# Kernel optimization log

Measured on AMD Instinct MI355X. Metric: run time of the kernel, lower is better.

## Reference

```python
import jax, jax.numpy as jnp
import numpy as np
import math

D_MODEL = 1024
EXPAND = 2
D_INNER = EXPAND * D_MODEL  # 2048
D_STATE = 16
D_CONV = 4
DT_RANK = math.ceil(D_MODEL / 16)  # 64
BATCH = 1
SEQLEN = 2048


def _silu(x):
    return x * jax.nn.sigmoid(x)


def _selective_scan(u, delta, A, B, C, D, z, delta_bias):
    """u, delta, z: (b,d,l); A: (d,n); B, C: (b,n,l); D, delta_bias: (d)."""
    delta = jax.nn.softplus(delta + delta_bias[None, :, None])        # (b,d,l)
    dA = jnp.exp(jnp.einsum('bdl,dn->lbdn', delta, A))                # (l,b,d,n)
    dBu = jnp.einsum('bdl,bnl->lbdn', delta * u, B)                   # (l,b,d,n)
    Ct = jnp.transpose(C, (2, 0, 1))                                  # (l,b,n)

    def step(h, inp):
        dA_t, dBu_t, C_t = inp
        h = dA_t * h + dBu_t                                          # (b,d,n)
        y = jnp.einsum('bdn,bn->bd', h, C_t)
        return h, y

    h0 = jnp.zeros((u.shape[0], u.shape[1], A.shape[1]), dtype=u.dtype)
    _, ys = jax.lax.scan(step, h0, (dA, dBu, Ct))                     # ys: (l,b,d)
    y = jnp.transpose(ys, (1, 2, 0))                                  # (b,d,l)
    y = y + D[:, None] * u
    return y * _silu(z)


def _causal_conv1d(x, conv_w, conv_b):
    """x: (b,d,l); conv_w: (d,w); conv_b: (d). Depthwise causal conv."""
    x_pad = jnp.pad(x, ((0, 0), (0, 0), (D_CONV - 1, 0)))
    kernel = conv_w[:, None, :]  # (d, 1, w)
    y = jax.lax.conv_general_dilated(
        x_pad, kernel, window_strides=(1,), padding='VALID',
        dimension_numbers=('NCH', 'OIH', 'NCH'),
        feature_group_count=D_INNER)
    return y + conv_b[None, :, None]


def setup_inputs() -> dict:
    key = jax.random.key(0)
    ks = jax.random.split(key, 12)
    hidden_states = jax.random.normal(ks[0], (BATCH, SEQLEN, D_MODEL), dtype=jnp.float32)
    in_proj_w = jax.random.normal(ks[1], (2 * D_INNER, D_MODEL), dtype=jnp.float32) * (D_MODEL ** -0.5)
    conv_w = jax.random.normal(ks[2], (D_INNER, D_CONV), dtype=jnp.float32) * (D_CONV ** -0.5)
    conv_b = jnp.zeros((D_INNER,), dtype=jnp.float32)
    dt_std = DT_RANK ** -0.5

    def dt_bias(k):
        dt = jnp.exp(jax.random.uniform(k, (D_INNER,)) * (math.log(0.1) - math.log(0.001)) + math.log(0.001))
        dt = jnp.clip(dt, 1e-4, None)
        return dt + jnp.log(-jnp.expm1(-dt))  # inverse softplus

    A_log = jnp.log(jnp.broadcast_to(jnp.arange(1, D_STATE + 1, dtype=jnp.float32), (D_INNER, D_STATE)))
    x1_proj_w = jax.random.normal(ks[3], (DT_RANK + 2 * D_STATE, D_INNER), dtype=jnp.float32) * (D_INNER ** -0.5)
    dt1_proj_w = jax.random.uniform(ks[4], (D_INNER, DT_RANK), minval=-dt_std, maxval=dt_std)
    dt1_proj_b = dt_bias(ks[5])
    x2_proj_w = jax.random.normal(ks[6], (DT_RANK + 2 * D_STATE, D_INNER), dtype=jnp.float32) * (D_INNER ** -0.5)
    dt2_proj_w = jax.random.uniform(ks[7], (D_INNER, DT_RANK), minval=-dt_std, maxval=dt_std)
    dt2_proj_b = dt_bias(ks[8])
    out_proj_w = jax.random.normal(ks[9], (D_MODEL, D_INNER), dtype=jnp.float32) * (D_INNER ** -0.5)
    return {
        'hidden_states': hidden_states,
        'in_proj_w': in_proj_w, 'conv_w': conv_w, 'conv_b': conv_b,
        'x1_proj_w': x1_proj_w, 'dt1_proj_w': dt1_proj_w, 'dt1_proj_b': dt1_proj_b,
        'A1_log': A_log, 'D1': jnp.ones((D_INNER,), dtype=jnp.float32),
        'x2_proj_w': x2_proj_w, 'dt2_proj_w': dt2_proj_w, 'dt2_proj_b': dt2_proj_b,
        'A2_log': A_log, 'D2': jnp.ones((D_INNER,), dtype=jnp.float32),
        'out_proj_w': out_proj_w,
    }


def reference(hidden_states, in_proj_w, conv_w, conv_b,
              x1_proj_w, dt1_proj_w, dt1_proj_b, A1_log, D1,
              x2_proj_w, dt2_proj_w, dt2_proj_b, A2_log, D2,
              out_proj_w):
    # in_proj: (b,l,d) @ W^T -> (b, 2*d_inner, l)
    xz = jnp.einsum('bld,ed->bel', hidden_states, in_proj_w)
    x, z = jnp.split(xz, 2, axis=1)                                   # (b,d_inner,l) each
    A1 = -jnp.exp(A1_log.astype(jnp.float32))
    A2 = -jnp.exp(A2_log.astype(jnp.float32))
    x = _silu(_causal_conv1d(x, conv_w, conv_b))                      # (b,d_inner,l)

    def branch_params(xp_w, dtp_w):
        dbl = jnp.einsum('bdl,kd->bkl', x, xp_w)                      # (b, r+2n, l)
        dt, Bm, Cm = jnp.split(dbl, [DT_RANK, DT_RANK + D_STATE], axis=1)
        dt = jnp.einsum('brl,dr->bdl', dt, dtp_w)
        return dt, Bm, Cm

    dt1, B1, C1 = branch_params(x1_proj_w, dt1_proj_w)
    dt2, B2, C2 = branch_params(x2_proj_w, dt2_proj_w)
    y1 = _selective_scan(x, dt1, A1, B1, C1, D1.astype(jnp.float32), z, dt1_proj_b.astype(jnp.float32))
    y2 = _selective_scan(x, dt2, A2, B2, C2, D2.astype(jnp.float32), z, dt2_proj_b.astype(jnp.float32))
    y = y1 - y2                                                       # (b,d_inner,l)
    out = jnp.einsum('bdl,od->blo', y, out_proj_w)                    # (b,l,d_model)
    return out
```

## Files before the change

kernel.cpp:

```cpp
#include <hip/hip_runtime.h>
#include <math.h>

#define SEQ 2048
#define DMODEL 1024
#define DIN 2048
#define NST 16
#define DTR 64
#define CH 64
#define NCH (SEQ / CH)

typedef __attribute__((ext_vector_type(8))) short bf16x8;
typedef __attribute__((ext_vector_type(4))) float f32x4;

__device__ __forceinline__ ushort f2bf(float f) {
  union { float f; unsigned u; } c; c.f = f;
  return (ushort)((c.u + 0x7fffu + ((c.u >> 16) & 1u)) >> 16);
}
__device__ __forceinline__ float bf2f(ushort h) {
  union { unsigned u; float f; } c; c.u = ((unsigned)h) << 16;
  return c.f;
}
__device__ __forceinline__ float splus(float v) {
  return v > 20.f ? v : log1pf(__expf(v));
}
__device__ __forceinline__ void powers16(float e, float* p) {
  float e2 = e * e, e4 = e2 * e2, e8 = e4 * e4;
  p[0] = e;       p[1] = e2;       p[2] = e2 * e;   p[3] = e4;
  p[4] = e4 * e;  p[5] = e4 * e2;  p[6] = e4 * p[2]; p[7] = e8;
  p[8] = e8 * e;  p[9] = e8 * e2;  p[10] = e8 * p[2]; p[11] = e8 * e4;
  p[12] = e8 * p[4]; p[13] = e8 * p[5]; p[14] = e8 * p[6]; p[15] = e8 * e8;
}

#define GLL(g, l) __builtin_amdgcn_global_load_lds( \
    (const __attribute__((address_space(1))) void*)(g), \
    (__attribute__((address_space(3))) void*)(l), 16, 0, 0)

template<int BM, int BN, int SPLITK, int MODE>
__global__ __launch_bounds__(256) void gemm3p(const ushort* __restrict__ Ahi,
                                              const ushort* __restrict__ Alo,
                                              const ushort* __restrict__ Bhi,
                                              const ushort* __restrict__ Blo,
                                              float* __restrict__ C,
                                              int M, int N, int K) {
  constexpr int BK = 32;
  constexpr int WM = BM / 2, WN = BN / 2, TM = WM / 16, TN = WN / 16;
  constexpr int SA = BM / 16, SB = BN / 16;
  constexpr bool dropB = (MODE == 2);
  __shared__ __align__(16) ushort sAh[BM * BK], sAl[BM * BK];
  __shared__ __align__(16) ushort sBh[BN * BK], sBl[BN * BK];
  const int tid = threadIdx.x, wid = tid >> 6, lane = tid & 63;
  const int m0 = blockIdx.y * BM, n0 = blockIdx.x * BN;
  const int Kc = K / SPLITK, kbeg = blockIdx.z * Kc;
  const int wm0 = (wid >> 1) * WM, wn0 = (wid & 1) * WN;
  const int fr = lane & 15;
  const int lrow = lane >> 2;
  const int lkc = (lane & 3) ^ ((lane >> 3) & 3);
  const int fpo = fr * 32 + (((lane >> 4) ^ ((lane >> 1) & 3)) * 8);

  f32x4 acc[TM][TN];
#pragma unroll
  for (int mi = 0; mi < TM; ++mi)
#pragma unroll
    for (int ni = 0; ni < TN; ++ni)
#pragma unroll
      for (int r = 0; r < 4; ++r) acc[mi][ni][r] = 0.f;

  for (int k0 = 0; k0 < Kc; k0 += BK) {
    __syncthreads();
    const int kg = kbeg + k0 + lkc * 8;
#pragma unroll
    for (int i = 0; i < SA / 4; ++i) {
      const int seg = wid * (SA / 4) + i;
      const size_t ga = (size_t)(m0 + seg * 16 + lrow) * K + kg;
      GLL(&Ahi[ga], &sAh[seg * 512]);
      GLL(&Alo[ga], &sAl[seg * 512]);
    }
#pragma unroll
    for (int i = 0; i < SB / 4; ++i) {
      const int seg = wid * (SB / 4) + i;
      const size_t ga = (size_t)(n0 + seg * 16 + lrow) * K + kg;
      GLL(&Bhi[ga], &sBh[seg * 512]);
      if (!dropB) GLL(&Blo[ga], &sBl[seg * 512]);
    }
    __syncthreads();

    bf16x8 ah[TM], al[TM], bh[TN], bl[TN];
#pragma unroll
    for (int mi = 0; mi < TM; ++mi) {
      const int r = (wm0 / 16 + mi) * 512 + fpo;
      ah[mi] = *(const bf16x8*)&sAh[r];
      al[mi] = *(const bf16x8*)&sAl[r];
    }
#pragma unroll
    for (int ni = 0; ni < TN; ++ni) {
      const int r = (wn0 / 16 + ni) * 512 + fpo;
      bh[ni] = *(const bf16x8*)&sBh[r];
      if (!dropB) bl[ni] = *(const bf16x8*)&sBl[r];
    }
#pragma unroll
    for (int mi = 0; mi < TM; ++mi)
#pragma unroll
      for (int ni = 0; ni < TN; ++ni) {
        acc[mi][ni] = __builtin_amdgcn_mfma_f32_16x16x32_bf16(ah[mi], bh[ni], acc[mi][ni], 0, 0, 0);
        if (!dropB)
          acc[mi][ni] = __builtin_amdgcn_mfma_f32_16x16x32_bf16(ah[mi], bl[ni], acc[mi][ni], 0, 0, 0);
        acc[mi][ni] = __builtin_amdgcn_mfma_f32_16x16x32_bf16(al[mi], bh[ni], acc[mi][ni], 0, 0, 0);
      }
  }

  float* __restrict__ Co = C + (size_t)blockIdx.z * M * N;
#pragma unroll
  for (int mi = 0; mi < TM; ++mi)
#pragma unroll
    for (int ni = 0; ni < TN; ++ni)
#pragma unroll
      for (int r = 0; r < 4; ++r)
        Co[(size_t)(m0 + wm0 + mi * 16 + (lane >> 4) * 4 + r) * N + n0 + wn0 + ni * 16 + fr] =
            acc[mi][ni][r];
}

__device__ __forceinline__ void split_store4(float4 v, ushort* hi, ushort* lo, size_t i) {
  ushort h0 = f2bf(v.x), h1 = f2bf(v.y), h2 = f2bf(v.z), h3 = f2bf(v.w);
  *(ushort4*)&hi[i] = make_ushort4(h0, h1, h2, h3);
  *(ushort4*)&lo[i] = make_ushort4(f2bf(v.x - bf2f(h0)), f2bf(v.y - bf2f(h1)),
                                   f2bf(v.z - bf2f(h2)), f2bf(v.w - bf2f(h3)));
}

__global__ __launch_bounds__(256) void cvt_fused(const float* __restrict__ inw,
                                                 const float* __restrict__ hid,
                                                 const float* __restrict__ x1w,
                                                 const float* __restrict__ x2w,
                                                 ushort* __restrict__ w_hi, ushort* __restrict__ w_lo,
                                                 ushort* __restrict__ h_hi, ushort* __restrict__ h_lo,
                                                 ushort* __restrict__ wx_hi, ushort* __restrict__ wx_lo) {
  const int q = blockIdx.x * 256 + threadIdx.x;
  const float* src; ushort* dhi; ushort* dlo; int base;
  if (q < 1048576)            { src = inw; dhi = w_hi;  dlo = w_lo;  base = q; }
  else if (q < 1572864)       { src = hid; dhi = h_hi;  dlo = h_lo;  base = q - 1048576; }
  else if (q < 1622016)       { src = x1w; dhi = wx_hi; dlo = wx_lo; base = q - 1572864; }
  else                        { src = x2w; dhi = wx_hi + 196608; dlo = wx_lo + 196608; base = q - 1622016; }
  const size_t i = (size_t)base * 4;
  split_store4(*(const float4*)&src[i], dhi, dlo, i);
}

__global__ __launch_bounds__(256) void reduce_out(const float* __restrict__ p,
                                                  float* __restrict__ o, int n) {
  const int i = (blockIdx.x * 256 + threadIdx.x) * 4;
  if (i >= n) return;
  float4 a = *(const float4*)&p[i];
  float4 b = *(const float4*)&p[(size_t)n + i];
  float4 c = *(const float4*)&p[(size_t)2 * n + i];
  float4 d = *(const float4*)&p[(size_t)3 * n + i];
  *(float4*)&o[i] = make_float4(a.x + b.x + c.x + d.x, a.y + b.y + c.y + d.y,
                                a.z + b.z + c.z + d.z, a.w + b.w + c.w + d.w);
}

__global__ __launch_bounds__(256) void conv_tr_kernel(const float* __restrict__ xz,
                                                      const float* __restrict__ cw,
                                                      const float* __restrict__ cb,
                                                      ushort* __restrict__ xcT_hi,
                                                      ushort* __restrict__ xcT_lo) {
  const int l0 = blockIdx.x * 64, d0 = blockIdx.y * 64;
  const int tid = threadIdx.x;
  __shared__ float xin[64][68];
  __shared__ float To[64][65];
  __shared__ float cwS[64][4];
  __shared__ float cbS[64];

  for (int i = tid; i < 1024; i += 256) {
    const int d = i >> 4, q = i & 15;
    float4 v = *(const float4*)&xz[(size_t)(d0 + d) * SEQ + l0 + q * 4];
    xin[d][3 + q * 4 + 0] = v.x; xin[d][3 + q * 4 + 1] = v.y;
    xin[d][3 + q * 4 + 2] = v.z; xin[d][3 + q * 4 + 3] = v.w;
  }
  if (tid < 192) {
    const int j = tid >> 6, d = tid & 63;
    const int l = l0 - 3 + j;
    xin[d][j] = (l >= 0) ? xz[(size_t)(d0 + d) * SEQ + l] : 0.f;
  }
  if (tid < 64) {
    cbS[tid] = cb[d0 + tid];
    float4 w = *(const float4*)&cw[(d0 + tid) * 4];
    cwS[tid][0] = w.x; cwS[tid][1] = w.y; cwS[tid][2] = w.z; cwS[tid][3] = w.w;
  }
  __syncthreads();

  for (int i = tid; i < 4096; i += 256) {
    const int d = i >> 6, l = i & 63;
    float a = cbS[d] + cwS[d][0] * xin[d][l] + cwS[d][1] * xin[d][l + 1] +
              cwS[d][2] * xin[d][l + 2] + cwS[d][3] * xin[d][l + 3];
    To[d][l] = a / (1.f + __expf(-a));
  }
  __syncthreads();

  for (int i = tid; i < 4096; i += 256) {
    const int l = i >> 6, dd = i & 63;
    float v = To[dd][l];
    ushort h = f2bf(v);
    xcT_hi[(size_t)(l0 + l) * DIN + d0 + dd] = h;
    xcT_lo[(size_t)(l0 + l) * DIN + d0 + dd] = f2bf(v - bf2f(h));
  }
}

__global__ __launch_bounds__(256) void ydiff_tr_kernel(const float* __restrict__ y1,
                                                       const float* __restrict__ y2,
                                                       const float* __restrict__ xz,
                                                       ushort* __restrict__ hi,
                                                       ushort* __restrict__ lo) {
  const int l0 = blockIdx.x * 64, d0 = blockIdx.y * 64;
  const int tid = threadIdx.x;
  __shared__ float Tz[64][65];
  for (int i = tid; i < 1024; i += 256) {
    const int d = i >> 4, q = i & 15;
    float4 v = *(const float4*)&xz[(size_t)(DIN + d0 + d) * SEQ + l0 + q * 4];
    Tz[d][q * 4 + 0] = v.x / (1.f + __expf(-v.x));
    Tz[d][q * 4 + 1] = v.y / (1.f + __expf(-v.y));
    Tz[d][q * 4 + 2] = v.z / (1.f + __expf(-v.z));
    Tz[d][q * 4 + 3] = v.w / (1.f + __expf(-v.w));
  }
  __syncthreads();
  for (int i = tid; i < 1024; i += 256) {
    const int l = i >> 4, dc = (i & 15) * 4;
    const size_t g = (size_t)(l0 + l) * DIN + d0 + dc;
    float4 a = *(const float4*)&y1[g];
    float4 b = *(const float4*)&y2[g];
    float4 v = make_float4((a.x - b.x) * Tz[dc + 0][l], (a.y - b.y) * Tz[dc + 1][l],
                           (a.z - b.z) * Tz[dc + 2][l], (a.w - b.w) * Tz[dc + 3][l]);
    split_store4(v, hi, lo, g);
  }
}

__global__ __launch_bounds__(256) void reduce_dblS_kernel(const float* __restrict__ p,
                                                          float* __restrict__ o,
                                                          float* __restrict__ BT1,
                                                          float* __restrict__ CT1,
                                                          float* __restrict__ BT2,
                                                          float* __restrict__ CT2) {
  const int NE = 192 * SEQ;
  const int idx = blockIdx.x * 256 + threadIdx.x;
  float s = 0.f;
#pragma unroll
  for (int cc = 0; cc < 8; ++cc) s += p[(size_t)cc * NE + idx];
  o[idx] = s;
  const int k = idx >> 11, l = idx & (SEQ - 1);
  if (k >= 64 && k < 80)        BT1[l * NST + (k - 64)] = s;
  else if (k >= 80 && k < 96)   CT1[l * NST + (k - 80)] = s;
  else if (k >= 160 && k < 176) BT2[l * NST + (k - 160)] = s;
  else if (k >= 176)            CT2[l * NST + (k - 176)] = s;
}

__global__ __launch_bounds__(256) void dt_gemm_kernel(const float* __restrict__ dbl1,
                                                      const float* __restrict__ dbl2,
                                                      const float* __restrict__ w1,
                                                      const float* __restrict__ w2,
                                                      const float* __restrict__ b1,
                                                      const float* __restrict__ b2,
                                                      float* __restrict__ o1,
                                                      float* __restrict__ o2) {
  const int br = blockIdx.z;
  const float* __restrict__ dbl = br ? dbl2 : dbl1;
  const float* __restrict__ W = br ? w2 : w1;
  const float* __restrict__ dtb = br ? b2 : b1;
  float* __restrict__ outp = br ? o2 : o1;
  const int l0 = blockIdx.x * 64, d0 = blockIdx.y * 64;
  __shared__ __align__(16) float Wt[64][68];
  __shared__ __align__(16) float Bs[64][68];
  const int tid = threadIdx.x;
  for (int i = tid; i < 4096; i += 256) {
    int a = i >> 6, b = i & 63;
    Wt[b][a] = W[(size_t)(d0 + a) * DTR + b];
    Bs[a][b] = dbl[(size_t)a * SEQ + l0 + b];
  }
  __syncthreads();
  const int tl_ = tid >> 4, td_ = tid & 15;
  float acc[4][4];
#pragma unroll
  for (int i = 0; i < 4; ++i)
#pragma unroll
    for (int j = 0; j < 4; ++j) acc[i][j] = 0.f;
  for (int r = 0; r < 64; ++r) {
    float4 av = *(const float4*)&Bs[r][tl_ * 4];
    float4 bv = *(const float4*)&Wt[r][td_ * 4];
    float am[4] = {av.x, av.y, av.z, av.w};
    float bn[4] = {bv.x, bv.y, bv.z, bv.w};
#pragma unroll
    for (int i = 0; i < 4; ++i)
#pragma unroll
      for (int j = 0; j < 4; ++j) acc[i][j] = fmaf(am[i], bn[j], acc[i][j]);
  }
  const float4 bias4 = *(const float4*)&dtb[d0 + td_ * 4];
#pragma unroll
  for (int i = 0; i < 4; ++i) {
    float4 w = make_float4(splus(acc[i][0] + bias4.x), splus(acc[i][1] + bias4.y),
                           splus(acc[i][2] + bias4.z), splus(acc[i][3] + bias4.w));
    *(float4*)&outp[(size_t)(l0 + tl_ * 4 + i) * DIN + d0 + td_ * 4] = w;
  }
}

__global__ __launch_bounds__(256) void scan_phase_a(const ushort* __restrict__ uhi,
                                                    const ushort* __restrict__ ulo,
                                                    const float* __restrict__ sp1T,
                                                    const float* __restrict__ sp2T,
                                                    const float* __restrict__ BT1,
                                                    const float* __restrict__ BT2,
                                                    const float* __restrict__ Al1,
                                                    const float* __restrict__ Al2,
                                                    float* __restrict__ hend,
                                                    float* __restrict__ Pend) {
  const int br = blockIdx.z;
  const float* __restrict__ spp = br ? sp2T : sp1T;
  const float* __restrict__ BT = br ? BT2 : BT1;
  const float* __restrict__ Al = br ? Al2 : Al1;
  const int c = blockIdx.y;
  const int t0 = c * CH;
  const int d = blockIdx.x * 256 + threadIdx.x;
  const size_t gbase = (size_t)t0 * DIN + d;

  __shared__ __align__(16) float Bs[CH][NST];
  ((float4*)Bs)[threadIdx.x] = ((const float4*)&BT[t0 * NST])[threadIdx.x];
  __syncthreads();

  bool fast = true;
#pragma unroll
  for (int n = 0; n < NST; ++n) {
    float kx = __expf(Al[(size_t)d * NST + n]);
    fast = fast && (fabsf(kx - (float)(n + 1)) < 1e-3f);
  }
  float h[NST];
#pragma unroll
  for (int n = 0; n < NST; ++n) h[n] = 0.f;
  float S = 0.f;

  if (fast) {
    for (int tt = 0; tt < CH / 4; ++tt) {
      float sparr[4], uarr[4];
#pragma unroll
      for (int j = 0; j < 4; ++j) {
        const size_t idx = gbase + (size_t)(tt * 4 + j) * DIN;
        sparr[j] = spp[idx];
        uarr[j] = bf2f(uhi[idx]) + bf2f(ulo[idx]);
      }
#pragma unroll
      for (int j = 0; j < 4; ++j) {
        const int t = tt * 4 + j;
        const float sp = sparr[j];
        S += sp;
        const float spu = sp * uarr[j];
        const float e = __expf(-sp);
        float p[NST];
        powers16(e, p);
#pragma unroll
        for (int ng = 0; ng < 4; ++ng) {
          float4 bq = *(const float4*)&Bs[t][ng * 4];
          float bf[4] = {bq.x, bq.y, bq.z, bq.w};
#pragma unroll
          for (int k = 0; k < 4; ++k) {
            int n = ng * 4 + k;
            h[n] = fmaf(p[n], h[n], spu * bf[k]);
          }
        }
      }
    }
  } else {
    float AnL2[NST];
#pragma unroll
    for (int n = 0; n < NST; ++n)
      AnL2[n] = -__expf(Al[(size_t)d * NST + n]) * 1.4426950408889634f;
    for (int tt = 0; tt < CH / 4; ++tt) {
      float sparr[4], uarr[4];
#pragma unroll
      for (int j = 0; j < 4; ++j) {
        const size_t idx = gbase + (size_t)(tt * 4 + j) * DIN;
        sparr[j] = spp[idx];
        uarr[j] = bf2f(uhi[idx]) + bf2f(ulo[idx]);
      }
#pragma unroll
      for (int j = 0; j < 4; ++j) {
        const int t = tt * 4 + j;
        const float sp = sparr[j];
        S += sp;
        const float spu = sp * uarr[j];
#pragma unroll
        for (int ng = 0; ng < 4; ++ng) {
          float4 bq = *(const float4*)&Bs[t][ng * 4];
          float bf[4] = {bq.x, bq.y, bq.z, bq.w};
#pragma unroll
          for (int k = 0; k < 4; ++k) {
            int n = ng * 4 + k;
            float dA = exp2f(AnL2[n] * sp);
            h[n] = fmaf(dA, h[n], spu * bf[k]);
          }
        }
      }
    }
  }

  float P[NST];
  if (fast) {
    powers16(__expf(-S), P);
  } else {
#pragma unroll
    for (int n = 0; n < NST; ++n)
      P[n] = exp2f(-__expf(Al[(size_t)d * NST + n]) * 1.4426950408889634f * S);
  }
  size_t base = ((size_t)(br * NCH + c) * DIN + d) * NST;
#pragma unroll
  for (int n = 0; n < NST; n += 4) {
    *(float4*)&hend[base + n] = make_float4(h[n], h[n + 1], h[n + 2], h[n + 3]);
    *(float4*)&Pend[base + n] = make_float4(P[n], P[n + 1], P[n + 2], P[n + 3]);
  }
}

__global__ __launch_bounds__(256) void carry_cvt(const float* __restrict__ hend,
                                                 float* __restrict__ PendHin,
                                                 const float* __restrict__ outw,
                                                 ushort* __restrict__ ow_hi) {
  const int b = blockIdx.x;
  if (b < 256) {
    const int flat = b * 256 + threadIdx.x;
    const int br = flat >> 15;
    const int dn = flat & 32767;
    float h = 0.f;
    for (int c = 0; c < NCH; ++c) {
      size_t idx = ((size_t)(br * NCH + c) << 15) + dn;
      float Pv = PendHin[idx];
      float he = hend[idx];
      PendHin[idx] = h;
      h = fmaf(Pv, h, he);
    }
  } else {
    const size_t i = ((size_t)(b - 256) * 256 + threadIdx.x) * 4;
    float4 v = *(const float4*)&outw[i];
    *(ushort4*)&ow_hi[i] = make_ushort4(f2bf(v.x), f2bf(v.y), f2bf(v.z), f2bf(v.w));
  }
}

__global__ __launch_bounds__(256) void scan_phase_c(const ushort* __restrict__ uhi,
                                                    const ushort* __restrict__ ulo,
                                                    const float* __restrict__ sp1T,
                                                    const float* __restrict__ sp2T,
                                                    const float* __restrict__ BT1,
                                                    const float* __restrict__ CT1,
                                                    const float* __restrict__ BT2,
                                                    const float* __restrict__ CT2,
                                                    const float* __restrict__ Al1,
                                                    const float* __restrict__ Al2,
                                                    const float* __restrict__ D1,
                                                    const float* __restrict__ D2,
                                                    const float* __restrict__ hin,
                                                    float* __restrict__ y1t,
                                                    float* __restrict__ y2t) {
  const int br = blockIdx.z;
  const float* __restrict__ spp = br ? sp2T : sp1T;
  const float* __restrict__ BT = br ? BT2 : BT1;
  const float* __restrict__ CT = br ? CT2 : CT1;
  const float* __restrict__ Al = br ? Al2 : Al1;
  const float* __restrict__ Dp = br ? D2 : D1;
  float* __restrict__ yt = br ? y2t : y1t;
  const int c = blockIdx.y;
  const int t0 = c * CH;
  const int d = blockIdx.x * 256 + threadIdx.x;
  const size_t gbase = (size_t)t0 * DIN + d;

  __shared__ __align__(16) float Bs[CH][NST];
  __shared__ __align__(16) float Cs[CH][NST];
  ((float4*)Bs)[threadIdx.x] = ((const float4*)&BT[t0 * NST])[threadIdx.x];
  ((float4*)Cs)[threadIdx.x] = ((const float4*)&CT[t0 * NST])[threadIdx.x];
  __syncthreads();

  bool fast = true;
#pragma unroll
  for (int n = 0; n < NST; ++n) {
    float kx = __expf(Al[(size_t)d * NST + n]);
    fast = fast && (fabsf(kx - (float)(n + 1)) < 1e-3f);
  }
  const float Dd = Dp[d];
  float h[NST];
  const size_t hbase = ((size_t)(br * NCH + c) * DIN + d) * NST;
#pragma unroll
  for (int n = 0; n < NST; n += 4) {
    float4 hv = *(const float4*)&hin[hbase + n];
    h[n] = hv.x; h[n + 1] = hv.y; h[n + 2] = hv.z; h[n + 3] = hv.w;
  }

  if (fast) {
    for (int tt = 0; tt < CH / 4; ++tt) {
      float sparr[4], uarr[4];
#pragma unroll
      for (int j = 0; j < 4; ++j) {
        const size_t idx = gbase + (size_t)(tt * 4 + j) * DIN;
        sparr[j] = spp[idx];
        uarr[j] = bf2f(uhi[idx]) + bf2f(ulo[idx]);
      }
#pragma unroll
      for (int j = 0; j < 4; ++j) {
        const int t = tt * 4 + j;
        const float sp = sparr[j];
        const float spu = sp * uarr[j];
        const float e = __expf(-sp);
        float p[NST];
        powers16(e, p);
        float y = 0.f;
#pragma unroll
        for (int ng = 0; ng < 4; ++ng) {
          float4 bq = *(const float4*)&Bs[t][ng * 4];
          float4 cq = *(const float4*)&Cs[t][ng * 4];
          float bf[4] = {bq.x, bq.y, bq.z, bq.w};
          float cf[4] = {cq.x, cq.y, cq.z, cq.w};
#pragma unroll
          for (int k = 0; k < 4; ++k) {
            int n = ng * 4 + k;
            h[n] = fmaf(p[n], h[n], spu * bf[k]);
            y = fmaf(h[n], cf[k], y);
          }
        }
        yt[gbase + (size_t)t * DIN] = y + Dd * uarr[j];
      }
    }
  } else {
    float AnL2[NST];
#pragma unroll
    for (int n = 0; n < NST; ++n)
      AnL2[n] = -__expf(Al[(size_t)d * NST + n]) * 1.4426950408889634f;
    for (int tt = 0; tt < CH / 4; ++tt) {
      float sparr[4], uarr[4];
#pragma unroll
      for (int j = 0; j < 4; ++j) {
        const size_t idx = gbase + (size_t)(tt * 4 + j) * DIN;
        sparr[j] = spp[idx];
        uarr[j] = bf2f(uhi[idx]) + bf2f(ulo[idx]);
      }
#pragma unroll
      for (int j = 0; j < 4; ++j) {
        const int t = tt * 4 + j;
        const float sp = sparr[j];
        const float spu = sp * uarr[j];
        float y = 0.f;
#pragma unroll
        for (int ng = 0; ng < 4; ++ng) {
          float4 bq = *(const float4*)&Bs[t][ng * 4];
          float4 cq = *(const float4*)&Cs[t][ng * 4];
          float bf[4] = {bq.x, bq.y, bq.z, bq.w};
          float cf[4] = {cq.x, cq.y, cq.z, cq.w};
#pragma unroll
          for (int k = 0; k < 4; ++k) {
            int n = ng * 4 + k;
            float dA = exp2f(AnL2[n] * sp);
            h[n] = fmaf(dA, h[n], spu * bf[k]);
            y = fmaf(h[n], cf[k], y);
          }
        }
        yt[gbase + (size_t)t * DIN] = y + Dd * uarr[j];
      }
    }
  }
}

extern "C" void kernel_launch(void* const* d_in, const int* in_sizes, int n_in,
                              void* d_out, int out_size, void* d_ws, size_t ws_size,
                              hipStream_t stream) {
  const float* hidden = (const float*)d_in[0];
  const float* in_proj_w = (const float*)d_in[1];
  const float* conv_w = (const float*)d_in[2];
  const float* conv_b = (const float*)d_in[3];
  const float* x1w = (const float*)d_in[4];
  const float* dtw1 = (const float*)d_in[5];
  const float* dtb1 = (const float*)d_in[6];
  const float* Al1 = (const float*)d_in[7];
  const float* D1 = (const float*)d_in[8];
  const float* x2w = (const float*)d_in[9];
  const float* dtw2 = (const float*)d_in[10];
  const float* dtb2 = (const float*)d_in[11];
  const float* Al2 = (const float*)d_in[12];
  const float* D2 = (const float*)d_in[13];
  const float* outw = (const float*)d_in[14];
  float* out = (float*)d_out;

  float* ws = (float*)d_ws;
  float* xz = ws;
  float* xcTbuf = xz + (size_t)4096 * SEQ;
  float* dblS = xcTbuf + (size_t)SEQ * DIN;
  float* sp1T = dblS + (size_t)192 * SEQ;
  float* sp2T = sp1T + (size_t)SEQ * DIN;
  float* y1t = sp2T + (size_t)SEQ * DIN;
  float* y2t = y1t + (size_t)SEQ * DIN;
  float* hend = y2t + (size_t)SEQ * DIN;
  float* Pend = hend + (size_t)2 * NCH * DIN * NST;
  float* BT1 = Pend + (size_t)2 * NCH * DIN * NST;
  float* CT1 = BT1 + (size_t)SEQ * NST;
  float* BT2 = CT1 + (size_t)SEQ * NST;
  float* CT2 = BT2 + (size_t)SEQ * NST;
  float* wxp = CT2 + (size_t)SEQ * NST;

  float* dbl1 = dblS;
  float* dbl2 = dblS + (size_t)96 * SEQ;

  ushort* xcT_hi = (ushort*)xcTbuf;
  ushort* xcT_lo = (ushort*)(xcTbuf + 2097152);
  ushort* w_hi = (ushort*)y1t;
  ushort* w_lo = (ushort*)(y1t + 2097152);
  ushort* h_hi = (ushort*)y2t;
  ushort* h_lo = (ushort*)(y2t + 1048576);
  ushort* wx_hi = (ushort*)wxp;
  ushort* wx_lo = (ushort*)(wxp + 196608);
  float* xp_part = sp1T;
  ushort* yd_hi = (ushort*)xcTbuf;
  ushort* yd_lo = (ushort*)(xcTbuf + 2097152);
  ushort* ow_hi = (ushort*)xz;
  float* opart = sp1T;

  dim3 blk(256);

  cvt_fused<<<dim3(6528), blk, 0, stream>>>(in_proj_w, hidden, x1w, x2w,
                                            w_hi, w_lo, h_hi, h_lo, wx_hi, wx_lo);

  gemm3p<128, 128, 1, 0><<<dim3(SEQ / 128, 4096 / 128, 1), blk, 0, stream>>>(
      w_hi, w_lo, h_hi, h_lo, xz, 4096, SEQ, DMODEL);

  conv_tr_kernel<<<dim3(SEQ / 64, DIN / 64), blk, 0, stream>>>(
      xz, conv_w, conv_b, xcT_hi, xcT_lo);

  gemm3p<64, 128, 8, 0><<<dim3(SEQ / 128, 192 / 64, 8), blk, 0, stream>>>(
      wx_hi, wx_lo, xcT_hi, xcT_lo, xp_part, 192, SEQ, DIN);

  reduce_dblS_kernel<<<dim3(192 * SEQ / 256), blk, 0, stream>>>(
      xp_part, dblS, BT1, CT1, BT2, CT2);

  dt_gemm_kernel<<<dim3(SEQ / 64, DIN / 64, 2), blk, 0, stream>>>(
      dbl1, dbl2, dtw1, dtw2, dtb1, dtb2, sp1T, sp2T);

  scan_phase_a<<<dim3(DIN / 256, NCH, 2), blk, 0, stream>>>(
      xcT_hi, xcT_lo, sp1T, sp2T, BT1, BT2, Al1, Al2, hend, Pend);
  carry_cvt<<<dim3(2304), blk, 0, stream>>>(hend, Pend, outw, ow_hi);
  scan_phase_c<<<dim3(DIN / 256, NCH, 2), blk, 0, stream>>>(
      xcT_hi, xcT_lo, sp1T, sp2T, BT1, CT1, BT2, CT2, Al1, Al2, D1, D2, Pend, y1t, y2t);

  ydiff_tr_kernel<<<dim3(SEQ / 64, DIN / 64), blk, 0, stream>>>(
      y1t, y2t, xz, yd_hi, yd_lo);

  gemm3p<128, 128, 4, 2><<<dim3(DMODEL / 128, SEQ / 128, 4), blk, 0, stream>>>(
      yd_hi, yd_lo, ow_hi, ow_hi, opart, SEQ, DMODEL, DIN);
  reduce_out<<<dim3(SEQ * DMODEL / 1024), blk, 0, stream>>>(opart, out, SEQ * DMODEL);
}
```

Before: 327.1 us.

## Switch split-precision GEMMs to fp16 with scaled residuals and fuse scan branches

Replaces the bf16 hi/lo split with fp16 hi plus a residual scaled by 2048, accumulated separately, and drops the low part of the hidden-state operand in the in_proj GEMM (MODE 2), which removes one MFMA per tile step. It also moves the silu(z) transpose into the conv kernel and fuses both scan branches into one thread, so the y-difference, gating and hi/lo split happen inside scan_phase_c and the ydiff kernel goes away. The scan chunk length is halved to expose more parallelism, and the GEMM gets a launch-bounds occupancy hint. These changes cut kernel launches, memory traffic and MFMA count, but fp16 has a narrower range than bf16 and dropping the activation residual may reduce accuracy.

```diff
diff --git a/kernel.cpp b/kernel.cpp
--- a/kernel.cpp
+++ b/kernel.cpp
@@ -6,19 +6,18 @@
 #define DIN 2048
 #define NST 16
 #define DTR 64
-#define CH 64
+#define CH 32
 #define NCH (SEQ / CH)
-
-typedef __attribute__((ext_vector_type(8))) short bf16x8;
+#define LOG2E 1.4426950408889634f
+
+typedef __attribute__((ext_vector_type(8))) _Float16 f16x8;
 typedef __attribute__((ext_vector_type(4))) float f32x4;
 
-__device__ __forceinline__ ushort f2bf(float f) {
-  union { float f; unsigned u; } c; c.f = f;
-  return (ushort)((c.u + 0x7fffu + ((c.u >> 16) & 1u)) >> 16);
-}
-__device__ __forceinline__ float bf2f(ushort h) {
-  union { unsigned u; float f; } c; c.u = ((unsigned)h) << 16;
-  return c.f;
+__device__ __forceinline__ ushort f2h(float f) {
+  union { _Float16 h; ushort u; } c; c.h = (_Float16)f; return c.u;
+}
+__device__ __forceinline__ float h2f(ushort u) {
+  union { ushort u; _Float16 h; } c; c.u = u; return (float)c.h;
 }
 __device__ __forceinline__ float splus(float v) {
   return v > 20.f ? v : log1pf(__expf(v));
@@ -36,18 +35,19 @@
     (__attribute__((address_space(3))) void*)(l), 16, 0, 0)
 
 template<int BM, int BN, int SPLITK, int MODE>
-__global__ __launch_bounds__(256) void gemm3p(const ushort* __restrict__ Ahi,
-                                              const ushort* __restrict__ Alo,
-                                              const ushort* __restrict__ Bhi,
-                                              const ushort* __restrict__ Blo,
-                                              float* __restrict__ C,
-                                              int M, int N, int K) {
+__global__ __launch_bounds__(256, 2) void gemm3p(const ushort* __restrict__ Ahi,
+                                                 const ushort* __restrict__ Alo,
+                                                 const ushort* __restrict__ Bhi,
+                                                 const ushort* __restrict__ Blo,
+                                                 float* __restrict__ C,
+                                                 int M, int N, int K) {
   constexpr int BK = 32;
   constexpr int WM = BM / 2, WN = BN / 2, TM = WM / 16, TN = WN / 16;
   constexpr int SA = BM / 16, SB = BN / 16;
   constexpr bool dropB = (MODE == 2);
   __shared__ __align__(16) ushort sAh[BM * BK], sAl[BM * BK];
-  __shared__ __align__(16) ushort sBh[BN * BK], sBl[BN * BK];
+  __shared__ __align__(16) ushort sBh[BN * BK];
+  __shared__ __align__(16) ushort sBl[dropB ? 16 : BN * BK];
   const int tid = threadIdx.x, wid = tid >> 6, lane = tid & 63;
   const int m0 = blockIdx.y * BM, n0 = blockIdx.x * BN;
   const int Kc = K / SPLITK, kbeg = blockIdx.z * Kc;
@@ -57,13 +57,13 @@
   const int lkc = (lane & 3) ^ ((lane >> 3) & 3);
   const int fpo = fr * 32 + (((lane >> 4) ^ ((lane >> 1) & 3)) * 8);
 
-  f32x4 acc[TM][TN];
+  f32x4 acc[TM][TN], accL[TM][TN];
 #pragma unroll
   for (int mi = 0; mi < TM; ++mi)
 #pragma unroll
     for (int ni = 0; ni < TN; ++ni)
 #pragma unroll
-      for (int r = 0; r < 4; ++r) acc[mi][ni][r] = 0.f;
+      for (int r = 0; r < 4; ++r) { acc[mi][ni][r] = 0.f; accL[mi][ni][r] = 0.f; }
 
   for (int k0 = 0; k0 < Kc; k0 += BK) {
     __syncthreads();
@@ -80,31 +80,31 @@
       const int seg = wid * (SB / 4) + i;
       const size_t ga = (size_t)(n0 + seg * 16 + lrow) * K + kg;
       GLL(&Bhi[ga], &sBh[seg * 512]);
-      if (!dropB) GLL(&Blo[ga], &sBl[seg * 512]);
+      if constexpr (!dropB) GLL(&Blo[ga], &sBl[seg * 512]);
     }
     __syncthreads();
 
-    bf16x8 ah[TM], al[TM], bh[TN], bl[TN];
+    f16x8 ah[TM], al[TM], bh[TN], bl[TN];
 #pragma unroll
     for (int mi = 0; mi < TM; ++mi) {
       const int r = (wm0 / 16 + mi) * 512 + fpo;
-      ah[mi] = *(const bf16x8*)&sAh[r];
-      al[mi] = *(const bf16x8*)&sAl[r];
+      ah[mi] = *(const f16x8*)&sAh[r];
+      al[mi] = *(const f16x8*)&sAl[r];
     }
 #pragma unroll
     for (int ni = 0; ni < TN; ++ni) {
       const int r = (wn0 / 16 + ni) * 512 + fpo;
-      bh[ni] = *(const bf16x8*)&sBh[r];
-      if (!dropB) bl[ni] = *(const bf16x8*)&sBl[r];
+      bh[ni] = *(const f16x8*)&sBh[r];
+      if constexpr (!dropB) bl[ni] = *(const f16x8*)&sBl[r];
     }
 #pragma unroll
     for (int mi = 0; mi < TM; ++mi)
 #pragma unroll
       for (int ni = 0; ni < TN; ++ni) {
-        acc[mi][ni] = __builtin_amdgcn_mfma_f32_16x16x32_bf16(ah[mi], bh[ni], acc[mi][ni], 0, 0, 0);
-        if (!dropB)
-          acc[mi][ni] = __builtin_amdgcn_mfma_f32_16x16x32_bf16(ah[mi], bl[ni], acc[mi][ni], 0, 0, 0);
-        acc[mi][ni] = __builtin_amdgcn_mfma_f32_16x16x32_bf16(al[mi], bh[ni], acc[mi][ni], 0, 0, 0);
+        acc[mi][ni] = __builtin_amdgcn_mfma_f32_16x16x32_f16(ah[mi], bh[ni], acc[mi][ni], 0, 0, 0);
+        accL[mi][ni] = __builtin_amdgcn_mfma_f32_16x16x32_f16(al[mi], bh[ni], accL[mi][ni], 0, 0, 0);
+        if constexpr (!dropB)
+          accL[mi][ni] = __builtin_amdgcn_mfma_f32_16x16x32_f16(ah[mi], bl[ni], accL[mi][ni], 0, 0, 0);
       }
   }
 
@@ -116,14 +116,14 @@
 #pragma unroll
       for (int r = 0; r < 4; ++r)
         Co[(size_t)(m0 + wm0 + mi * 16 + (lane >> 4) * 4 + r) * N + n0 + wn0 + ni * 16 + fr] =
-            acc[mi][ni][r];
-}
-
-__device__ __forceinline__ void split_store4(float4 v, ushort* hi, ushort* lo, size_t i) {
-  ushort h0 = f2bf(v.x), h1 = f2bf(v.y), h2 = f2bf(v.z), h3 = f2bf(v.w);
+            acc[mi][ni][r] + accL[mi][ni][r] * (1.f / 2048.f);
+}
+
+__device__ __forceinline__ void split_store4h(float4 v, ushort* hi, ushort* lo, size_t i) {
+  ushort h0 = f2h(v.x), h1 = f2h(v.y), h2 = f2h(v.z), h3 = f2h(v.w);
   *(ushort4*)&hi[i] = make_ushort4(h0, h1, h2, h3);
-  *(ushort4*)&lo[i] = make_ushort4(f2bf(v.x - bf2f(h0)), f2bf(v.y - bf2f(h1)),
-                                   f2bf(v.z - bf2f(h2)), f2bf(v.w - bf2f(h3)));
+  *(ushort4*)&lo[i] = make_ushort4(f2h((v.x - h2f(h0)) * 2048.f), f2h((v.y - h2f(h1)) * 2048.f),
+                                   f2h((v.z - h2f(h2)) * 2048.f), f2h((v.w - h2f(h3)) * 2048.f));
 }
 
 __global__ __launch_bounds__(256) void cvt_fused(const float* __restrict__ inw,
@@ -131,16 +131,21 @@
                                                  const float* __restrict__ x1w,
                                                  const float* __restrict__ x2w,
                                                  ushort* __restrict__ w_hi, ushort* __restrict__ w_lo,
-                                                 ushort* __restrict__ h_hi, ushort* __restrict__ h_lo,
+                                                 ushort* __restrict__ h_hi,
                                                  ushort* __restrict__ wx_hi, ushort* __restrict__ wx_lo) {
   const int q = blockIdx.x * 256 + threadIdx.x;
+  if (q >= 1048576 && q < 1572864) {
+    const size_t i = (size_t)(q - 1048576) * 4;
+    float4 v = *(const float4*)&hid[i];
+    *(ushort4*)&h_hi[i] = make_ushort4(f2h(v.x), f2h(v.y), f2h(v.z), f2h(v.w));
+    return;
+  }
   const float* src; ushort* dhi; ushort* dlo; int base;
-  if (q < 1048576)            { src = inw; dhi = w_hi;  dlo = w_lo;  base = q; }
-  else if (q < 1572864)       { src = hid; dhi = h_hi;  dlo = h_lo;  base = q - 1048576; }
-  else if (q < 1622016)       { src = x1w; dhi = wx_hi; dlo = wx_lo; base = q - 1572864; }
-  else                        { src = x2w; dhi = wx_hi + 196608; dlo = wx_lo + 196608; base = q - 1622016; }
+  if (q < 1048576)       { src = inw; dhi = w_hi;  dlo = w_lo;  base = q; }
+  else if (q < 1622016)  { src = x1w; dhi = wx_hi; dlo = wx_lo; base = q - 1572864; }
+  else                   { src = x2w; dhi = wx_hi + 196608; dlo = wx_lo + 196608; base = q - 1622016; }
   const size_t i = (size_t)base * 4;
-  split_store4(*(const float4*)&src[i], dhi, dlo, i);
+  split_store4h(*(const float4*)&src[i], dhi, dlo, i);
 }
 
 __global__ __launch_bounds__(256) void reduce_out(const float* __restrict__ p,
@@ -159,7 +164,8 @@
                                                       const float* __restrict__ cw,
                                                       const float* __restrict__ cb,
                                                       ushort* __restrict__ xcT_hi,
-                                                      ushort* __restrict__ xcT_lo) {
+                                                      ushort* __restrict__ xcT_lo,
+                                                      float* __restrict__ zsT) {
   const int l0 = blockIdx.x * 64, d0 = blockIdx.y * 64;
   const int tid = threadIdx.x;
   __shared__ float xin[64][68];
@@ -196,37 +202,24 @@
   for (int i = tid; i < 4096; i += 256) {
     const int l = i >> 6, dd = i & 63;
     float v = To[dd][l];
-    ushort h = f2bf(v);
+    ushort h = f2h(v);
     xcT_hi[(size_t)(l0 + l) * DIN + d0 + dd] = h;
-    xcT_lo[(size_t)(l0 + l) * DIN + d0 + dd] = f2bf(v - bf2f(h));
-  }
-}
-
-__global__ __launch_bounds__(256) void ydiff_tr_kernel(const float* __restrict__ y1,
-                                                       const float* __restrict__ y2,
-                                                       const float* __restrict__ xz,
-                                                       ushort* __restrict__ hi,
-                                                       ushort* __restrict__ lo) {
-  const int l0 = blockIdx.x * 64, d0 = blockIdx.y * 64;
-  const int tid = threadIdx.x;
-  __shared__ float Tz[64][65];
+    xcT_lo[(size_t)(l0 + l) * DIN + d0 + dd] = f2h((v - h2f(h)) * 2048.f);
+  }
+  __syncthreads();
+
   for (int i = tid; i < 1024; i += 256) {
     const int d = i >> 4, q = i & 15;
     float4 v = *(const float4*)&xz[(size_t)(DIN + d0 + d) * SEQ + l0 + q * 4];
-    Tz[d][q * 4 + 0] = v.x / (1.f + __expf(-v.x));
-    Tz[d][q * 4 + 1] = v.y / (1.f + __expf(-v.y));
-    Tz[d][q * 4 + 2] = v.z / (1.f + __expf(-v.z));
-    Tz[d][q * 4 + 3] = v.w / (1.f + __expf(-v.w));
+    To[d][q * 4 + 0] = v.x / (1.f + __expf(-v.x));
+    To[d][q * 4 + 1] = v.y / (1.f + __expf(-v.y));
+    To[d][q * 4 + 2] = v.z / (1.f + __expf(-v.z));
+    To[d][q * 4 + 3] = v.w / (1.f + __expf(-v.w));
   }
   __syncthreads();
-  for (int i = tid; i < 1024; i += 256) {
-    const int l = i >> 4, dc = (i & 15) * 4;
-    const size_t g = (size_t)(l0 + l) * DIN + d0 + dc;
-    float4 a = *(const float4*)&y1[g];
-    float4 b = *(const float4*)&y2[g];
-    float4 v = make_float4((a.x - b.x) * Tz[dc + 0][l], (a.y - b.y) * Tz[dc + 1][l],
-                           (a.z - b.z) * Tz[dc + 2][l], (a.w - b.w) * Tz[dc + 3][l]);
-    split_store4(v, hi, lo, g);
+  for (int i = tid; i < 4096; i += 256) {
+    const int l = i >> 6, dd = i & 63;
+    zsT[(size_t)(l0 + l) * DIN + d0 + dd] = To[dd][l];
   }
 }
 
@@ -307,107 +300,101 @@
                                                     const float* __restrict__ Al2,
                                                     float* __restrict__ hend,
                                                     float* __restrict__ Pend) {
-  const int br = blockIdx.z;
-  const float* __restrict__ spp = br ? sp2T : sp1T;
-  const float* __restrict__ BT = br ? BT2 : BT1;
-  const float* __restrict__ Al = br ? Al2 : Al1;
-  const int c = blockIdx.y;
-  const int t0 = c * CH;
+  const int c = blockIdx.y, t0 = c * CH;
   const int d = blockIdx.x * 256 + threadIdx.x;
   const size_t gbase = (size_t)t0 * DIN + d;
 
-  __shared__ __align__(16) float Bs[CH][NST];
-  ((float4*)Bs)[threadIdx.x] = ((const float4*)&BT[t0 * NST])[threadIdx.x];
+  __shared__ __align__(16) float Bs[2][CH][NST];
+  {
+    const int j = threadIdx.x;
+    if (j < 128) ((float4*)&Bs[0][0][0])[j] = ((const float4*)&BT1[(size_t)t0 * NST])[j];
+    else ((float4*)&Bs[1][0][0])[j - 128] = ((const float4*)&BT2[(size_t)t0 * NST])[j - 128];
+  }
   __syncthreads();
 
   bool fast = true;
 #pragma unroll
   for (int n = 0; n < NST; ++n) {
-    float kx = __expf(Al[(size_t)d * NST + n]);
-    fast = fast && (fabsf(kx - (float)(n + 1)) < 1e-3f);
-  }
-  float h[NST];
-#pragma unroll
-  for (int n = 0; n < NST; ++n) h[n] = 0.f;
-  float S = 0.f;
+    float k1 = __expf(Al1[(size_t)d * NST + n]);
+    float k2 = __expf(Al2[(size_t)d * NST + n]);
+    fast = fast && (fabsf(k1 - (float)(n + 1)) < 1e-3f) && (fabsf(k2 - (float)(n + 1)) < 1e-3f);
+  }
+  float h1[NST], h2[NST];
+#pragma unroll
+  for (int n = 0; n < NST; ++n) { h1[n] = 0.f; h2[n] = 0.f; }
+  float S1 = 0.f, S2 = 0.f;
 
   if (fast) {
     for (int tt = 0; tt < CH / 4; ++tt) {
-      float sparr[4], uarr[4];
+      float s1[4], s2[4], ua[4];
 #pragma unroll
       for (int j = 0; j < 4; ++j) {
         const size_t idx = gbase + (size_t)(tt * 4 + j) * DIN;
-        sparr[j] = spp[idx];
-        uarr[j] = bf2f(uhi[idx]) + bf2f(ulo[idx]);
+        s1[j] = sp1T[idx]; s2[j] = sp2T[idx];
+        ua[j] = h2f(uhi[idx]) + h2f(ulo[idx]) * (1.f / 2048.f);
       }
 #pragma unroll
       for (int j = 0; j < 4; ++j) {
         const int t = tt * 4 + j;
-        const float sp = sparr[j];
-        S += sp;
-        const float spu = sp * uarr[j];
-        const float e = __expf(-sp);
+        S1 += s1[j]; S2 += s2[j];
+        const float spu1 = s1[j] * ua[j], spu2 = s2[j] * ua[j];
         float p[NST];
-        powers16(e, p);
-#pragma unroll
-        for (int ng = 0; ng < 4; ++ng) {
-          float4 bq = *(const float4*)&Bs[t][ng * 4];
-          float bf[4] = {bq.x, bq.y, bq.z, bq.w};
-#pragma unroll
-          for (int k = 0; k < 4; ++k) {
-            int n = ng * 4 + k;
-            h[n] = fmaf(p[n], h[n], spu * bf[k]);
-          }
+        powers16(__expf(-s1[j]), p);
+#pragma unroll
+        for (int n = 0; n < NST; ++n) h1[n] = fmaf(p[n], h1[n], spu1 * Bs[0][t][n]);
+        powers16(__expf(-s2[j]), p);
+#pragma unroll
+        for (int n = 0; n < NST; ++n) h2[n] = fmaf(p[n], h2[n], spu2 * Bs[1][t][n]);
+      }
+    }
+  } else {
+    float A1e[NST], A2e[NST];
+#pragma unroll
+    for (int n = 0; n < NST; ++n) {
+      A1e[n] = -__expf(Al1[(size_t)d * NST + n]) * LOG2E;
+      A2e[n] = -__expf(Al2[(size_t)d * NST + n]) * LOG2E;
+    }
+    for (int tt = 0; tt < CH / 4; ++tt) {
+      float s1[4], s2[4], ua[4];
+#pragma unroll
+      for (int j = 0; j < 4; ++j) {
+        const size_t idx = gbase + (size_t)(tt * 4 + j) * DIN;
+        s1[j] = sp1T[idx]; s2[j] = sp2T[idx];
+        ua[j] = h2f(uhi[idx]) + h2f(ulo[idx]) * (1.f / 2048.f);
+      }
+#pragma unroll
+      for (int j = 0; j < 4; ++j) {
+        const int t = tt * 4 + j;
+        S1 += s1[j]; S2 += s2[j];
+        const float spu1 = s1[j] * ua[j], spu2 = s2[j] * ua[j];
+#pragma unroll
+        for (int n = 0; n < NST; ++n) {
+          h1[n] = fmaf(exp2f(A1e[n] * s1[j]), h1[n], spu1 * Bs[0][t][n]);
+          h2[n] = fmaf(exp2f(A2e[n] * s2[j]), h2[n], spu2 * Bs[1][t][n]);
         }
       }
     }
+  }
+
+  float P1[NST], P2[NST];
+  if (fast) {
+    powers16(__expf(-S1), P1);
+    powers16(__expf(-S2), P2);
   } else {
-    float AnL2[NST];
-#pragma unroll
-    for (int n = 0; n < NST; ++n)
-      AnL2[n] = -__expf(Al[(size_t)d * NST + n]) * 1.4426950408889634f;
-    for (int tt = 0; tt < CH / 4; ++tt) {
-      float sparr[4], uarr[4];
-#pragma unroll
-      for (int j = 0; j < 4; ++j) {
-        const size_t idx = gbase + (size_t)(tt * 4 + j) * DIN;
-        sparr[j] = spp[idx];
-        uarr[j] = bf2f(uhi[idx]) + bf2f(ulo[idx]);
-      }
-#pragma unroll
-      for (int j = 0; j < 4; ++j) {
-        const int t = tt * 4 + j;
-        const float sp = sparr[j];
-        S += sp;
-        const float spu = sp * uarr[j];
-#pragma unroll
-        for (int ng = 0; ng < 4; ++ng) {
-          float4 bq = *(const float4*)&Bs[t][ng * 4];
-          float bf[4] = {bq.x, bq.y, bq.z, bq.w};
-#pragma unroll
-          for (int k = 0; k < 4; ++k) {
-            int n = ng * 4 + k;
-            float dA = exp2f(AnL2[n] * sp);
-            h[n] = fmaf(dA, h[n], spu * bf[k]);
-          }
-        }
-      }
-    }
-  }
-
-  float P[NST];
-  if (fast) {
-    powers16(__expf(-S), P);
-  } else {
-#pragma unroll
-    for (int n = 0; n < NST; ++n)
-      P[n] = exp2f(-__expf(Al[(size_t)d * NST + n]) * 1.4426950408889634f * S);
-  }
-  size_t base = ((size_t)(br * NCH + c) * DIN + d) * NST;
+#pragma unroll
+    for (int n = 0; n < NST; ++n) {
+      P1[n] = exp2f(-__expf(Al1[(size_t)d * NST + n]) * LOG2E * S1);
+      P2[n] = exp2f(-__expf(Al2[(size_t)d * NST + n]) * LOG2E * S2);
+    }
+  }
+  const size_t b1 = ((size_t)c * DIN + d) * NST;
+  const size_t b2 = ((size_t)(NCH + c) * DIN + d) * NST;
 #pragma unroll
   for (int n = 0; n < NST; n += 4) {
-    *(float4*)&hend[base + n] = make_float4(h[n], h[n + 1], h[n + 2], h[n + 3]);
-    *(float4*)&Pend[base + n] = make_float4(P[n], P[n + 1], P[n + 2], P[n + 3]);
+    *(float4*)&hend[b1 + n] = make_float4(h1[n], h1[n + 1], h1[n + 2], h1[n + 3]);
+    *(float4*)&Pend[b1 + n] = make_float4(P1[n], P1[n + 1], P1[n + 2], P1[n + 3]);
+    *(float4*)&hend[b2 + n] = make_float4(h2[n], h2[n + 1], h2[n + 2], h2[n + 3]);
+    *(float4*)&Pend[b2 + n] = make_float4(P2[n], P2[n + 1], P2[n + 2], P2[n + 3]);
   }
 }
 
@@ -431,7 +418,7 @@
   } else {
     const size_t i = ((size_t)(b - 256) * 256 + threadIdx.x) * 4;
     float4 v = *(const float4*)&outw[i];
-    *(ushort4*)&ow_hi[i] = make_ushort4(f2bf(v.x), f2bf(v.y), f2bf(v.z), f2bf(v.w));
+    *(ushort4*)&ow_hi[i] = make_ushort4(f2h(v.x), f2h(v.y), f2h(v.z), f2h(v.w));
   }
 }
 
@@ -448,109 +435,112 @@
                                                     const float* __restrict__ D1,
                                                     const float* __restrict__ D2,
                                                     const float* __restrict__ hin,
-                                                    float* __restrict__ y1t,
-                                                    float* __restrict__ y2t) {
-  const int br = blockIdx.z;
-  const float* __restrict__ spp = br ? sp2T : sp1T;
-  const float* __restrict__ BT = br ? BT2 : BT1;
-  const float* __restrict__ CT = br ? CT2 : CT1;
-  const float* __restrict__ Al = br ? Al2 : Al1;
-  const float* __restrict__ Dp = br ? D2 : D1;
-  float* __restrict__ yt = br ? y2t : y1t;
-  const int c = blockIdx.y;
-  const int t0 = c * CH;
+                                                    const float* __restrict__ zsT,
+                                                    ushort* __restrict__ yd_hi,
+                                                    ushort* __restrict__ yd_lo) {
+  const int c = blockIdx.y, t0 = c * CH;
   const int d = blockIdx.x * 256 + threadIdx.x;
   const size_t gbase = (size_t)t0 * DIN + d;
 
-  __shared__ __align__(16) float Bs[CH][NST];
-  __shared__ __align__(16) float Cs[CH][NST];
-  ((float4*)Bs)[threadIdx.x] = ((const float4*)&BT[t0 * NST])[threadIdx.x];
-  ((float4*)Cs)[threadIdx.x] = ((const float4*)&CT[t0 * NST])[threadIdx.x];
+  __shared__ __align__(16) float Bs[2][CH][NST];
+  __shared__ __align__(16) float Cs[2][CH][NST];
+  {
+    const int j = threadIdx.x;
+    if (j < 128) {
+      ((float4*)&Bs[0][0][0])[j] = ((const float4*)&BT1[(size_t)t0 * NST])[j];
+      ((float4*)&Cs[0][0][0])[j] = ((const float4*)&CT1[(size_t)t0 * NST])[j];
+    } else {
+      ((float4*)&Bs[1][0][0])[j - 128] = ((const float4*)&BT2[(size_t)t0 * NST])[j - 128];
+      ((float4*)&Cs[1][0][0])[j - 128] = ((const float4*)&CT2[(size_t)t0 * NST])[j - 128];
+    }
+  }
   __syncthreads();
 
   bool fast = true;
 #pragma unroll
   for (int n = 0; n < NST; ++n) {
-    float kx = __expf(Al[(size_t)d * NST + n]);
-    fast = fast && (fabsf(kx - (float)(n + 1)) < 1e-3f);
-  }
-  const float Dd = Dp[d];
-  float h[NST];
-  const size_t hbase = ((size_t)(br * NCH + c) * DIN + d) * NST;
+    float k1 = __expf(Al1[(size_t)d * NST + n]);
+    float k2 = __expf(Al2[(size_t)d * NST + n]);
+    fast = fast && (fabsf(k1 - (float)(n + 1)) < 1e-3f) && (fabsf(k2 - (float)(n + 1)) < 1e-3f);
+  }
+  const float Ddd = D1[d] - D2[d];
+  float h1[NST], h2[NST];
+  const size_t hb1 = ((size_t)c * DIN + d) * NST;
+  const size_t hb2 = ((size_t)(NCH + c) * DIN + d) * NST;
 #pragma unroll
   for (int n = 0; n < NST; n += 4) {
-    float4 hv = *(const float4*)&hin[hbase + n];
-    h[n] = hv.x; h[n + 1] = hv.y; h[n + 2] = hv.z; h[n + 3] = hv.w;
+    float4 v1 = *(const float4*)&hin[hb1 + n];
+    h1[n] = v1.x; h1[n + 1] = v1.y; h1[n + 2] = v1.z; h1[n + 3] = v1.w;
+    float4 v2 = *(const float4*)&hin[hb2 + n];
+    h2[n] = v2.x; h2[n + 1] = v2.y; h2[n + 2] = v2.z; h2[n + 3] = v2.w;
   }
 
   if (fast) {
     for (int tt = 0; tt < CH / 4; ++tt) {
-      float sparr[4], uarr[4];
+      float s1[4], s2[4], ua[4];
 #pragma unroll
       for (int j = 0; j < 4; ++j) {
         const size_t idx = gbase + (size_t)(tt * 4 + j) * DIN;
-        sparr[j] = spp[idx];
-        uarr[j] = bf2f(uhi[idx]) + bf2f(ulo[idx]);
+        s1[j] = sp1T[idx]; s2[j] = sp2T[idx];
+        ua[j] = h2f(uhi[idx]) + h2f(ulo[idx]) * (1.f / 2048.f);
       }
 #pragma unroll
       for (int j = 0; j < 4; ++j) {
         const int t = tt * 4 + j;
-        const float sp = sparr[j];
-        const float spu = sp * uarr[j];
-        const float e = __expf(-sp);
+        const size_t idx = gbase + (size_t)t * DIN;
+        const float spu1 = s1[j] * ua[j], spu2 = s2[j] * ua[j];
         float p[NST];
-        powers16(e, p);
-        float y = 0.f;
-#pragma unroll
-        for (int ng = 0; ng < 4; ++ng) {
-          float4 bq = *(const float4*)&Bs[t][ng * 4];
-          float4 cq = *(const float4*)&Cs[t][ng * 4];
-          float bf[4] = {bq.x, bq.y, bq.z, bq.w};
-          float cf[4] = {cq.x, cq.y, cq.z, cq.w};
-#pragma unroll
-          for (int k = 0; k < 4; ++k) {
-            int n = ng * 4 + k;
-            h[n] = fmaf(p[n], h[n], spu * bf[k]);
-            y = fmaf(h[n], cf[k], y);
-          }
+        float y1 = 0.f, y2 = 0.f;
+        powers16(__expf(-s1[j]), p);
+#pragma unroll
+        for (int n = 0; n < NST; ++n) {
+          h1[n] = fmaf(p[n], h1[n], spu1 * Bs[0][t][n]);
+          y1 = fmaf(h1[n], Cs[0][t][n], y1);
         }
-        yt[gbase + (size_t)t * DIN] = y + Dd * uarr[j];
+        powers16(__expf(-s2[j]), p);
+#pragma unroll
+        for (int n = 0; n < NST; ++n) {
+          h2[n] = fmaf(p[n], h2[n], spu2 * Bs[1][t][n]);
+          y2 = fmaf(h2[n], Cs[1][t][n], y2);
+        }
+        const float yd = (y1 - y2 + Ddd * ua[j]) * zsT[idx];
+        const ushort hh = f2h(yd);
+        yd_hi[idx] = hh;
+        yd_lo[idx] = f2h((yd - h2f(hh)) * 2048.f);
       }
     }
   } else {
-    float AnL2[NST];
-#pragma unroll
-    for (int n = 0; n < NST; ++n)
-      AnL2[n] = -__expf(Al[(size_t)d * NST + n]) * 1.4426950408889634f;
+    float A1e[NST], A2e[NST];
+#pragma unroll
+    for (int n = 0; n < NST; ++n) {
+      A1e[n] = -__expf(Al1[(size_t)d * NST + n]) * LOG2E;
+      A2e[n] = -__expf(Al2[(size_t)d * NST + n]) * LOG2E;
+    }
     for (int tt = 0; tt < CH / 4; ++tt) {
-      float sparr[4], uarr[4];
+      float s1[4], s2[4], ua[4];
 #pragma unroll
       for (int j = 0; j < 4; ++j) {
         const size_t idx = gbase + (size_t)(tt * 4 + j) * DIN;
-        sparr[j] = spp[idx];
-        uarr[j] = bf2f(uhi[idx]) + bf2f(ulo[idx]);
+        s1[j] = sp1T[idx]; s2[j] = sp2T[idx];
+        ua[j] = h2f(uhi[idx]) + h2f(ulo[idx]) * (1.f / 2048.f);
       }
 #pragma unroll
       for (int j = 0; j < 4; ++j) {
         const int t = tt * 4 + j;
-        const float sp = sparr[j];
-        const float spu = sp * uarr[j];
-        float y = 0.f;
-#pragma unroll
-        for (int ng = 0; ng < 4; ++ng) {
-          float4 bq = *(const float4*)&Bs[t][ng * 4];
-          float4 cq = *(const float4*)&Cs[t][ng * 4];
-          float bf[4] = {bq.x, bq.y, bq.z, bq.w};
-          float cf[4] = {cq.x, cq.y, cq.z, cq.w};
-#pragma unroll
-          for (int k = 0; k < 4; ++k) {
-            int n = ng * 4 + k;
-            float dA = exp2f(AnL2[n] * sp);
-            h[n] = fmaf(dA, h[n], spu * bf[k]);
-            y = fmaf(h[n], cf[k], y);
-          }
+        const size_t idx = gbase + (size_t)t * DIN;
+        const float spu1 = s1[j] * ua[j], spu2 = s2[j] * ua[j];
+        float y1 = 0.f, y2 = 0.f;
+#pragma unroll
+        for (int n = 0; n < NST; ++n) {
+          h1[n] = fmaf(exp2f(A1e[n] * s1[j]), h1[n], spu1 * Bs[0][t][n]);
+          y1 = fmaf(h1[n], Cs[0][t][n], y1);
+          h2[n] = fmaf(exp2f(A2e[n] * s2[j]), h2[n], spu2 * Bs[1][t][n]);
+          y2 = fmaf(h2[n], Cs[1][t][n], y2);
         }
-        yt[gbase + (size_t)t * DIN] = y + Dd * uarr[j];
+        const float yd = (y1 - y2 + Ddd * ua[j]) * zsT[idx];
+        const ushort hh = f2h(yd);
+        yd_hi[idx] = hh;
+        yd_lo[idx] = f2h((yd - h2f(hh)) * 2048.f);
       }
     }
   }
@@ -582,11 +572,10 @@
   float* dblS = xcTbuf + (size_t)SEQ * DIN;
   float* sp1T = dblS + (size_t)192 * SEQ;
   float* sp2T = sp1T + (size_t)SEQ * DIN;
-  float* y1t = sp2T + (size_t)SEQ * DIN;
-  float* y2t = y1t + (size_t)SEQ * DIN;
-  float* hend = y2t + (size_t)SEQ * DIN;
-  float* Pend = hend + (size_t)2 * NCH * DIN * NST;
-  float* BT1 = Pend + (size_t)2 * NCH * DIN * NST;
+  float* siluzT = sp2T + (size_t)SEQ * DIN;
+  float* hendB = siluzT + (size_t)SEQ * DIN;
+  float* PendB = hendB + (size_t)2 * NCH * DIN * NST;
+  float* BT1 = PendB + (size_t)2 * NCH * DIN * NST;
   float* CT1 = BT1 + (size_t)SEQ * NST;
   float* BT2 = CT1 + (size_t)SEQ * NST;
   float* CT2 = BT2 + (size_t)SEQ * NST;
@@ -597,10 +586,9 @@
 
   ushort* xcT_hi = (ushort*)xcTbuf;
   ushort* xcT_lo = (ushort*)(xcTbuf + 2097152);
-  ushort* w_hi = (ushort*)y1t;
-  ushort* w_lo = (ushort*)(y1t + 2097152);
-  ushort* h_hi = (ushort*)y2t;
-  ushort* h_lo = (ushort*)(y2t + 1048576);
+  ushort* w_hi = (ushort*)siluzT;
+  ushort* w_lo = (ushort*)(siluzT + 2097152);
+  ushort* h_hi = (ushort*)hendB;
   ushort* wx_hi = (ushort*)wxp;
   ushort* wx_lo = (ushort*)(wxp + 196608);
   float* xp_part = sp1T;
@@ -612,13 +600,13 @@
   dim3 blk(256);
 
   cvt_fused<<<dim3(6528), blk, 0, stream>>>(in_proj_w, hidden, x1w, x2w,
-                                            w_hi, w_lo, h_hi, h_lo, wx_hi, wx_lo);
-
-  gemm3p<128, 128, 1, 0><<<dim3(SEQ / 128, 4096 / 128, 1), blk, 0, stream>>>(
-      w_hi, w_lo, h_hi, h_lo, xz, 4096, SEQ, DMODEL);
+                                            w_hi, w_lo, h_hi, wx_hi, wx_lo);
+
+  gemm3p<128, 128, 1, 2><<<dim3(SEQ / 128, 4096 / 128, 1), blk, 0, stream>>>(
+      w_hi, w_lo, h_hi, h_hi, xz, 4096, SEQ, DMODEL);
 
   conv_tr_kernel<<<dim3(SEQ / 64, DIN / 64), blk, 0, stream>>>(
-      xz, conv_w, conv_b, xcT_hi, xcT_lo);
+      xz, conv_w, conv_b, xcT_hi, xcT_lo, siluzT);
 
   gemm3p<64, 128, 8, 0><<<dim3(SEQ / 128, 192 / 64, 8), blk, 0, stream>>>(
       wx_hi, wx_lo, xcT_hi, xcT_lo, xp_part, 192, SEQ, DIN);
@@ -629,14 +617,12 @@
   dt_gemm_kernel<<<dim3(SEQ / 64, DIN / 64, 2), blk, 0, stream>>>(
       dbl1, dbl2, dtw1, dtw2, dtb1, dtb2, sp1T, sp2T);
 
-  scan_phase_a<<<dim3(DIN / 256, NCH, 2), blk, 0, stream>>>(
-      xcT_hi, xcT_lo, sp1T, sp2T, BT1, BT2, Al1, Al2, hend, Pend);
-  carry_cvt<<<dim3(2304), blk, 0, stream>>>(hend, Pend, outw, ow_hi);
-  scan_phase_c<<<dim3(DIN / 256, NCH, 2), blk, 0, stream>>>(
-      xcT_hi, xcT_lo, sp1T, sp2T, BT1, CT1, BT2, CT2, Al1, Al2, D1, D2, Pend, y1t, y2t);
-
-  ydiff_tr_kernel<<<dim3(SEQ / 64, DIN / 64), blk, 0, stream>>>(
-      y1t, y2t, xz, yd_hi, yd_lo);
+  scan_phase_a<<<dim3(DIN / 256, NCH), blk, 0, stream>>>(
+      xcT_hi, xcT_lo, sp1T, sp2T, BT1, BT2, Al1, Al2, hendB, PendB);
+  carry_cvt<<<dim3(2304), blk, 0, stream>>>(hendB, PendB, outw, ow_hi);
+  scan_phase_c<<<dim3(DIN / 256, NCH), blk, 0, stream>>>(
+      xcT_hi, xcT_lo, sp1T, sp2T, BT1, CT1, BT2, CT2, Al1, Al2, D1, D2,
+      PendB, siluzT, yd_hi, yd_lo);
 
   gemm3p<128, 128, 4, 2><<<dim3(DMODEL / 128, SEQ / 128, 4), blk, 0, stream>>>(
       yd_hi, yd_lo, ow_hi, ow_hi, opart, SEQ, DMODEL, DIN);
```

After: 332.5 us. Within noise of the previous version (+1.6%).
